# Optimization experiments

Hardware: AMD Instinct MI355X
Metric: run time of the kernel (lower is better)

Reference implementation:

```python
import jax, jax.numpy as jnp
import numpy as np
from jax import lax

K = 7            # pool_size / PSROI_BINS
C_OUT = 10       # output channels per bin (features has K*K*C_OUT channels)
FEAT_STRIDE = 16
LAMDA = 0.1
SAMPLES = 2      # bilinear sample points per bin side
H = W = 200
C_IN = K * K * C_OUT  # 490
N_ROIS = 512


def setup_inputs() -> dict:
    key = jax.random.key(0)
    k1, k2, k3, k4 = jax.random.split(key, 4)
    features = jax.random.normal(k1, (1, H, W, C_IN), jnp.float32)
    conv_w = jax.random.truncated_normal(k2, -2.0, 2.0, (3, 3, C_IN, 2 * K * K), jnp.float32) * 0.01
    img = H * FEAT_STRIDE  # image-space extent
    cxy = jax.random.uniform(k3, (N_ROIS, 2), minval=0.0, maxval=img - 1.0)
    wh = jax.random.uniform(k4, (N_ROIS, 2), minval=64.0, maxval=640.0)
    x1 = jnp.clip(cxy[:, 0] - wh[:, 0] * 0.5, 0.0, img - 2.0)
    y1 = jnp.clip(cxy[:, 1] - wh[:, 1] * 0.5, 0.0, img - 2.0)
    x2 = jnp.clip(x1 + wh[:, 0], x1 + 1.0, img - 1.0)
    y2 = jnp.clip(y1 + wh[:, 1], y1 + 1.0, img - 1.0)
    rois = jnp.stack([jnp.zeros(N_ROIS), x1, y1, x2, y2], axis=-1)  # [N,5]
    return {"features": features, "rois": rois, "conv_w": conv_w}


def _bilinear(feat, y, x):
    """feat [H,W,C]; y,x arbitrary equal shapes -> [..., C]."""
    Hf, Wf = feat.shape[0], feat.shape[1]
    y = jnp.clip(y, 0.0, Hf - 1.0)
    x = jnp.clip(x, 0.0, Wf - 1.0)
    y0 = jnp.floor(y)
    x0 = jnp.floor(x)
    y0i = y0.astype(jnp.int32)
    x0i = x0.astype(jnp.int32)
    y1i = jnp.minimum(y0i + 1, Hf - 1)
    x1i = jnp.minimum(x0i + 1, Wf - 1)
    wy = (y - y0)[..., None]
    wx = (x - x0)[..., None]
    v00 = feat[y0i, x0i]
    v01 = feat[y0i, x1i]
    v10 = feat[y1i, x0i]
    v11 = feat[y1i, x1i]
    return (v00 * (1 - wy) * (1 - wx) + v01 * (1 - wy) * wx
            + v10 * wy * (1 - wx) + v11 * wy * wx)


def _ps_roi(feat, box, cpg, offsets):
    """Position-sensitive RoI avg pooling with optional per-bin offsets.
    feat [H,W,K*K*cpg]; box (x1,y1,x2,y2) image coords; offsets [K,K,2] (dx,dy)
    in image coords or None. Returns [K,K,cpg]."""
    x1, y1, x2, y2 = box
    fx1 = x1 / FEAT_STRIDE
    fy1 = y1 / FEAT_STRIDE
    bw = (x2 - x1 + 1.0) / FEAT_STRIDE / K
    bh = (y2 - y1 + 1.0) / FEAT_STRIDE / K
    idx = jnp.arange(K, dtype=feat.dtype)
    s = (jnp.arange(SAMPLES, dtype=feat.dtype) + 0.5) / SAMPLES
    sx = fx1 + (idx[:, None] + s[None, :]) * bw  # [K(j), S]
    sy = fy1 + (idx[:, None] + s[None, :]) * bh  # [K(i), S]
    gx = jnp.broadcast_to(sx[None, :, None, :], (K, K, SAMPLES, SAMPLES))
    gy = jnp.broadcast_to(sy[:, None, :, None], (K, K, SAMPLES, SAMPLES))
    if offsets is not None:
        off = offsets / FEAT_STRIDE  # image -> feature coords
        gx = gx + off[..., 0][:, :, None, None]
        gy = gy + off[..., 1][:, :, None, None]
    vals = _bilinear(feat, gy, gx)                     # [K,K,S,S,K*K*cpg]
    vals = vals.reshape(K, K, SAMPLES, SAMPLES, K * K, cpg)
    bin_idx = (jnp.arange(K)[:, None] * K + jnp.arange(K)[None, :])  # [K,K]
    sel = jnp.take_along_axis(
        vals, bin_idx[:, :, None, None, None, None], axis=4)[..., 0, :]
    return sel.mean(axis=(2, 3))  # [K,K,cpg]


def reference(features, rois, conv_w):
    # 3x3 same conv producing 2*K*K offset channels (no bias)
    offset_map = lax.conv_general_dilated(
        features, conv_w, (1, 1), 'SAME',
        dimension_numbers=('NHWC', 'HWIO', 'NHWC'))[0]  # [H,W,2*K*K]
    feat0 = features[0]  # [H,W,K*K*C_OUT]

    def one_roi(roi):
        x1, y1, x2, y2 = roi[1], roi[2], roi[3], roi[4]
        rw = x2 - x1 + 1.0
        rh = y2 - y1 + 1.0
        box = (x1, y1, x2, y2)
        # stage 1: pool the offset map position-sensitively -> [K,K,2]
        off = _ps_roi(offset_map, box, 2, None).reshape(-1, 2)
        off = jnp.stack((off[:, 0] * rw * LAMDA,
                         off[:, 1] * rh * LAMDA), axis=-1).reshape(K, K, 2)
        # stage 2: deformable PS-RoI pooling of the features -> [K,K,C_OUT]
        return _ps_roi(feat0, box, C_OUT, off)

    return jax.vmap(one_roi)(rois)  # [N, K, K, C_OUT]
```

## Files before the change

### kernel.cpp

```cpp
#include <hip/hip_runtime.h>
#include <hip/hip_bf16.h>

#define Hh   200
#define Ww   200
#define CIN  490
#define OCN  98
#define KK   7
#define COUT 10
#define NROIS 512
#define PIX  8

#define PH   202
#define PW   202
#define PC   512
#define NPIX (Hh * Ww)
#define KCN  16
#define NF   7
#define NUNITS 144
#define HGRAN  18
#define HALF_SHORTS (8 * 3584)

typedef __attribute__((ext_vector_type(8))) short short8;
typedef __attribute__((ext_vector_type(4))) float float4v;

__global__ __launch_bounds__(256) void pack_feat_kernel(
    const float* __restrict__ feat, __hip_bfloat16* __restrict__ pf)
{
    int tid = blockIdx.x * 256 + threadIdx.x;
    if (tid >= PH * PW * (PC / 8)) return;
    int c8  = (tid & 63) * 8;
    int pix = tid >> 6;
    int py = pix / PW, px = pix % PW;
    __hip_bfloat16* dst = pf + (size_t)pix * PC + c8;
    bool interior = (py >= 1 && py <= Hh && px >= 1 && px <= Ww);

    __hip_bfloat16 v[8];
    if (interior && c8 + 8 <= CIN) {
        const float* s = feat + ((size_t)(py - 1) * Ww + (px - 1)) * CIN + c8;
#pragma unroll
        for (int q = 0; q < 4; ++q) {
            float2 f2 = *reinterpret_cast<const float2*>(s + q * 2);
            v[q * 2]     = __float2bfloat16(f2.x);
            v[q * 2 + 1] = __float2bfloat16(f2.y);
        }
    } else {
        const float* s = interior ? feat + ((size_t)(py - 1) * Ww + (px - 1)) * CIN : nullptr;
#pragma unroll
        for (int j = 0; j < 8; ++j) {
            float val = (interior && (c8 + j) < CIN) ? s[c8 + j] : 0.f;
            v[j] = __float2bfloat16(val);
        }
    }
    *reinterpret_cast<short8*>(dst) = *reinterpret_cast<short8*>(v);
}

__global__ __launch_bounds__(256) void pack_w_kernel(
    const float* __restrict__ w, __hip_bfloat16* __restrict__ bp)
{
    int idx = blockIdx.x * 256 + threadIdx.x;
    if (idx >= NUNITS * NF * 64 * 8) return;
    int j = idx & 7;
    int l = (idx >> 3) & 63;
    int f = (idx >> 9) % NF;
    int u = idx / (NF * 512);
    int kc = u / 9, tap = u % 9;
    int k = kc * 32 + ((l >> 4) * 8) + j;
    int n = f * 16 + (l & 15);
    float val = (k < CIN && n < OCN) ? w[((size_t)tap * CIN + k) * OCN + n] : 0.f;
    bp[idx] = __float2bfloat16(val);
}

__global__ __launch_bounds__(640) void conv_mfma_kernel(
    const short* __restrict__ pf,
    const short* __restrict__ bp,
    float* __restrict__ om)
{
    __shared__ short bsm[2 * HALF_SHORTS];

    int l = threadIdx.x & 63;
    int w = threadIdx.x >> 6;
    int mpos = w % 5;
    int ks = w / 5;
    int ubase = ks * 72;
    int m0 = blockIdx.x * 160 + mpos * 32;

    const short* abase0;
    const short* abase1;
    {
        int row0 = m0 + (l & 15);
        int row1 = m0 + 16 + (l & 15);
        int y0 = row0 / Ww, x0 = row0 % Ww;
        int y1 = row1 / Ww, x1 = row1 % Ww;
        abase0 = pf + ((size_t)(y0 * PW + x0) * PC) + ((l >> 4) * 8);
        abase1 = pf + ((size_t)(y1 * PW + x1) * PC) + ((l >> 4) * 8);
    }

    float4v acc[2][NF];
#pragma unroll
    for (int r = 0; r < 2; ++r)
#pragma unroll
        for (int f = 0; f < NF; ++f) acc[r][f] = (float4v){0.f, 0.f, 0.f, 0.f};

    auto aOff = [&](int u) -> int {
        int kc = u / 9, tap = u - kc * 9;
        int ky = tap / 3, kx = tap - ky * 3;
        return (ky * PW + kx) * PC + kc * 32;
    };
    int lbase = ks * HALF_SHORTS;

#pragma unroll
    for (int s = 0; s < 6; ++s) {
        int i = mpos + s * 5;
        if (i < 28) {
            int uu = ubase + i / 7, f = i % 7;
            short8 v = *reinterpret_cast<const short8*>(
                bp + ((size_t)(uu * NF + f)) * 512 + l * 8);
            *reinterpret_cast<short8*>(
                &bsm[lbase + (uu & 7) * 3584 + f * 512 + l * 8]) = v;
        }
    }
    short8 a00 = *reinterpret_cast<const short8*>(abase0 + aOff(ubase + 0));
    short8 a01 = *reinterpret_cast<const short8*>(abase0 + aOff(ubase + 1));
    short8 a02 = *reinterpret_cast<const short8*>(abase0 + aOff(ubase + 2));
    short8 a03 = *reinterpret_cast<const short8*>(abase0 + aOff(ubase + 3));
    short8 a10 = *reinterpret_cast<const short8*>(abase1 + aOff(ubase + 0));
    short8 a11 = *reinterpret_cast<const short8*>(abase1 + aOff(ubase + 1));
    short8 a12 = *reinterpret_cast<const short8*>(abase1 + aOff(ubase + 2));
    short8 a13 = *reinterpret_cast<const short8*>(abase1 + aOff(ubase + 3));
    __syncthreads();

    for (int g = 0; g < HGRAN; ++g) {
        bool more = (g < HGRAN - 1);
        int u0n = ubase + (g + 1) * 4;

        short8 st0, st1, st2, st3, st4, st5;
        int off0 = -1, off1 = -1, off2 = -1, off3 = -1, off4 = -1, off5 = -1;
        if (more) {
#define STAGE_LOAD(S, STV, OFFV)                                               \
            {                                                                  \
                int i = mpos + (S) * 5;                                        \
                if (i < 28) {                                                  \
                    int uu = u0n + i / 7, f = i % 7;                           \
                    STV = *reinterpret_cast<const short8*>(                    \
                        bp + ((size_t)(uu * NF + f)) * 512 + l * 8);           \
                    OFFV = lbase + (uu & 7) * 3584 + f * 512 + l * 8;          \
                }                                                              \
            }
            STAGE_LOAD(0, st0, off0)
            STAGE_LOAD(1, st1, off1)
            STAGE_LOAD(2, st2, off2)
            STAGE_LOAD(3, st3, off3)
            STAGE_LOAD(4, st4, off4)
            STAGE_LOAD(5, st5, off5)
#undef STAGE_LOAD
        }
        short8 n00, n01, n02, n03, n10, n11, n12, n13;
        if (more) {
            n00 = *reinterpret_cast<const short8*>(abase0 + aOff(u0n + 0));
            n01 = *reinterpret_cast<const short8*>(abase0 + aOff(u0n + 1));
            n02 = *reinterpret_cast<const short8*>(abase0 + aOff(u0n + 2));
            n03 = *reinterpret_cast<const short8*>(abase0 + aOff(u0n + 3));
            n10 = *reinterpret_cast<const short8*>(abase1 + aOff(u0n + 0));
            n11 = *reinterpret_cast<const short8*>(abase1 + aOff(u0n + 1));
            n12 = *reinterpret_cast<const short8*>(abase1 + aOff(u0n + 2));
            n13 = *reinterpret_cast<const short8*>(abase1 + aOff(u0n + 3));
        }

        int u0 = ubase + g * 4;
#define COMPUTE_UNIT(J, AR0, AR1)                                               \
        {                                                                       \
            int sbase = lbase + ((u0 + J) & 7) * 3584 + l * 8;                  \
            _Pragma("unroll")                                                   \
            for (int f = 0; f < NF; ++f) {                                      \
                short8 b = *reinterpret_cast<short8*>(&bsm[sbase + f * 512]);   \
                acc[0][f] = __builtin_amdgcn_mfma_f32_16x16x32_bf16(            \
                    AR0, b, acc[0][f], 0, 0, 0);                                \
                acc[1][f] = __builtin_amdgcn_mfma_f32_16x16x32_bf16(            \
                    AR1, b, acc[1][f], 0, 0, 0);                                \
            }                                                                   \
        }
        COMPUTE_UNIT(0, a00, a10)
        COMPUTE_UNIT(1, a01, a11)
        COMPUTE_UNIT(2, a02, a12)
        COMPUTE_UNIT(3, a03, a13)
#undef COMPUTE_UNIT

        if (off0 >= 0) *reinterpret_cast<short8*>(&bsm[off0]) = st0;
        if (off1 >= 0) *reinterpret_cast<short8*>(&bsm[off1]) = st1;
        if (off2 >= 0) *reinterpret_cast<short8*>(&bsm[off2]) = st2;
        if (off3 >= 0) *reinterpret_cast<short8*>(&bsm[off3]) = st3;
        if (off4 >= 0) *reinterpret_cast<short8*>(&bsm[off4]) = st4;
        if (off5 >= 0) *reinterpret_cast<short8*>(&bsm[off5]) = st5;
        if (more) {
            a00 = n00; a01 = n01; a02 = n02; a03 = n03;
            a10 = n10; a11 = n11; a12 = n12; a13 = n13;
        }
        __syncthreads();
    }

    float* lred = (float*)bsm;
    if (ks == 1) {
#pragma unroll
        for (int r = 0; r < 2; ++r)
#pragma unroll
            for (int f = 0; f < NF; ++f) {
                int idx = (((mpos * 2 + r) * NF + f) * 64 + l) * 4;
                *reinterpret_cast<float4v*>(&lred[idx]) = acc[r][f];
            }
    }
    __syncthreads();
    if (ks == 0) {
        int n = l & 15;
#pragma unroll
        for (int r = 0; r < 2; ++r) {
            int rbase = m0 + r * 16 + ((l >> 4) * 4);
#pragma unroll
            for (int f = 0; f < NF; ++f) {
                int idx = (((mpos * 2 + r) * NF + f) * 64 + l) * 4;
                float4v other = *reinterpret_cast<float4v*>(&lred[idx]);
                float4v tot = acc[r][f] + other;
                int col = f * 16 + n;
                if (col < OCN) {
#pragma unroll
                    for (int j = 0; j < 4; ++j)
                        om[(size_t)(rbase + j) * OCN + col] = tot[j];
                }
            }
        }
    }
}

__global__ __launch_bounds__(256) void conv3x3_kernel(
    const float* __restrict__ feat, const float* __restrict__ w,
    const float* __restrict__ zero, float* __restrict__ om)
{
    int idx = blockIdx.x * blockDim.x + threadIdx.x;
    if (idx >= Hh * (Ww / PIX) * OCN) return;
    int oc = idx % OCN;
    int g  = idx / OCN;
    int x0 = (g % (Ww / PIX)) * PIX;
    int y  = g / (Ww / PIX);

    float acc[PIX];
#pragma unroll
    for (int p = 0; p < PIX; ++p) acc[p] = 0.f;

    for (int ky = 0; ky < 3; ++ky) {
        int yy = y + ky - 1;
        if (yy < 0 || yy >= Hh) continue;
        const float* frow = feat + (size_t)yy * Ww * CIN;
        for (int kx = 0; kx < 3; ++kx) {
            const float* wp = w + ((ky * 3 + kx) * CIN) * OCN + oc;
            const float* fp[PIX];
#pragma unroll
            for (int p = 0; p < PIX; ++p) {
                int xx = x0 + p + kx - 1;
                fp[p] = (xx >= 0 && xx < Ww) ? (frow + (size_t)xx * CIN) : zero;
            }
            for (int ic = 0; ic < CIN; ic += 2) {
                float w0 = wp[ic * OCN];
                float w1 = wp[(ic + 1) * OCN];
#pragma unroll
                for (int p = 0; p < PIX; ++p) {
                    float2 f = *reinterpret_cast<const float2*>(fp[p] + ic);
                    acc[p] = fmaf(f.x, w0, acc[p]);
                    acc[p] = fmaf(f.y, w1, acc[p]);
                }
            }
        }
    }
    float* orow = om + ((size_t)y * Ww + x0) * OCN + oc;
#pragma unroll
    for (int p = 0; p < PIX; ++p) orow[p * OCN] = acc[p];
}

__device__ __forceinline__ void bilin_setup(float y, float x,
    int& i00, int& i01, int& i10, int& i11,
    float& w00, float& w01, float& w10, float& w11)
{
    y = fminf(fmaxf(y, 0.f), 199.f);
    x = fminf(fmaxf(x, 0.f), 199.f);
    float y0f = floorf(y), x0f = floorf(x);
    int y0 = (int)y0f, x0i = (int)x0f;
    int y1 = min(y0 + 1, 199), x1 = min(x0i + 1, 199);
    float wy = y - y0f, wx = x - x0f;
    i00 = y0 * Ww + x0i;  i01 = y0 * Ww + x1;
    i10 = y1 * Ww + x0i;  i11 = y1 * Ww + x1;
    w00 = (1.f - wy) * (1.f - wx);
    w01 = (1.f - wy) * wx;
    w10 = wy * (1.f - wx);
    w11 = wy * wx;
}

__global__ __launch_bounds__(256) void psroi_kernel(
    const float* __restrict__ feat, const float* __restrict__ rois,
    const float* __restrict__ om, float* __restrict__ out)
{
    int n = blockIdx.x;
    int t = threadIdx.x;

    float x1 = rois[n * 5 + 1], y1 = rois[n * 5 + 2];
    float x2 = rois[n * 5 + 3], y2 = rois[n * 5 + 4];
    float rw = x2 - x1 + 1.0f, rh = y2 - y1 + 1.0f;
    float fx1 = x1 * 0.0625f, fy1 = y1 * 0.0625f;
    float bw = (rw * 0.0625f) / 7.0f;
    float bh = (rh * 0.0625f) / 7.0f;

    __shared__ float offs[49][2];

    if (t < 49) {
        int bi = t / 7, bj = t % 7;
        float ax = 0.f, ay = 0.f;
#pragma unroll
        for (int ss = 0; ss < 4; ++ss) {
            float sj = ((float)(ss & 1) + 0.5f) * 0.5f;
            float si = ((float)(ss >> 1) + 0.5f) * 0.5f;
            float gx = fx1 + ((float)bj + sj) * bw;
            float gy = fy1 + ((float)bi + si) * bh;
            int i00, i01, i10, i11; float w00, w01, w10, w11;
            bilin_setup(gy, gx, i00, i01, i10, i11, w00, w01, w10, w11);
            int c0 = t * 2;
            const float* p00 = om + (size_t)i00 * OCN + c0;
            const float* p01 = om + (size_t)i01 * OCN + c0;
            const float* p10 = om + (size_t)i10 * OCN + c0;
            const float* p11 = om + (size_t)i11 * OCN + c0;
            ax += w00 * p00[0] + w01 * p01[0] + w10 * p10[0] + w11 * p11[0];
            ay += w00 * p00[1] + w01 * p01[1] + w10 * p10[1] + w11 * p11[1];
        }
        offs[t][0] = ax * 0.25f * rw * 0.1f * 0.0625f;
        offs[t][1] = ay * 0.25f * rh * 0.1f * 0.0625f;
    }
    __syncthreads();

    for (int o = t; o < KK * KK * COUT; o += blockDim.x) {
        int bin = o / COUT, c = o % COUT;
        int bi = bin / 7, bj = bin % 7;
        float dx = offs[bin][0], dy = offs[bin][1];
        int ch = bin * COUT + c;
        float acc = 0.f;
#pragma unroll
        for (int ss = 0; ss < 4; ++ss) {
            float sj = ((float)(ss & 1) + 0.5f) * 0.5f;
            float si = ((float)(ss >> 1) + 0.5f) * 0.5f;
            float gx = fx1 + ((float)bj + sj) * bw + dx;
            float gy = fy1 + ((float)bi + si) * bh + dy;
            int i00, i01, i10, i11; float w00, w01, w10, w11;
            bilin_setup(gy, gx, i00, i01, i10, i11, w00, w01, w10, w11);
            acc += w00 * feat[(size_t)i00 * CIN + ch]
                 + w01 * feat[(size_t)i01 * CIN + ch]
                 + w10 * feat[(size_t)i10 * CIN + ch]
                 + w11 * feat[(size_t)i11 * CIN + ch];
        }
        out[(size_t)n * (KK * KK * COUT) + o] = acc * 0.25f;
    }
}

extern "C" void kernel_launch(void* const* d_in, const int* in_sizes, int n_in,
                              void* d_out, int out_size, void* d_ws, size_t ws_size,
                              hipStream_t stream) {
    const float* feat = (const float*)d_in[0];
    const float* rois = (const float*)d_in[1];
    const float* w    = (const float*)d_in[2];
    float* out = (float*)d_out;

    const size_t OM_BYTES = (size_t)NPIX * OCN * 4;
    const size_t BP_BYTES = (size_t)NUNITS * NF * 64 * 8 * 2;
    const size_t PF_BYTES = (size_t)PH * PW * PC * 2;
    const size_t NEEDED = OM_BYTES + BP_BYTES + PF_BYTES;

    if (ws_size >= NEEDED) {
        float* om = (float*)d_ws;
        __hip_bfloat16* bp = (__hip_bfloat16*)((char*)d_ws + OM_BYTES);
        __hip_bfloat16* pf = (__hip_bfloat16*)((char*)d_ws + OM_BYTES + BP_BYTES);

        int wThreads = NUNITS * NF * 64 * 8;
        pack_w_kernel<<<(wThreads + 255) / 256, 256, 0, stream>>>(w, bp);
        int fThreads = PH * PW * (PC / 8);
        pack_feat_kernel<<<(fThreads + 255) / 256, 256, 0, stream>>>(feat, pf);
        conv_mfma_kernel<<<250, 640, 0, stream>>>(
            (const short*)pf, (const short*)bp, om);
        psroi_kernel<<<NROIS, 256, 0, stream>>>(feat, rois, om, out);
    } else {
        float* zero = (float*)d_ws;
        float* om   = (float*)d_ws + 1024;
        hipMemsetAsync(d_ws, 0, 4096, stream);
        int convThreads = Hh * (Ww / PIX) * OCN;
        conv3x3_kernel<<<(convThreads + 255) / 256, 256, 0, stream>>>(feat, w, zero, om);
        psroi_kernel<<<NROIS, 256, 0, stream>>>(feat, rois, om, out);
    }
}
```

Before: 108.6 us.

## Remap conv blocks per XCD, stream A-fragment loads, request two blocks per CU

The conv kernel now remaps blockIdx so that each XCD handles a contiguous range of row tiles, which is meant to improve L2 locality for the shared halo rows. The next A fragments are now loaded straight into the current registers right after each unit's MFMAs, replacing the separate prefetch register set, to cut VGPR pressure. The launch bounds now ask for a minimum of two blocks per CU. The shorter prefetch distance may expose more load latency, and the hard-coded 32/31 split assumes a grid of 250 blocks.

```diff
diff --git a/kernel.cpp b/kernel.cpp
--- a/kernel.cpp
+++ b/kernel.cpp
@@ -70,19 +70,24 @@
     bp[idx] = __float2bfloat16(val);
 }
 
-__global__ __launch_bounds__(640) void conv_mfma_kernel(
+__global__ __launch_bounds__(640, 2) void conv_mfma_kernel(
     const short* __restrict__ pf,
     const short* __restrict__ bp,
     float* __restrict__ om)
 {
     __shared__ short bsm[2 * HALF_SHORTS];
+
+    int orig = blockIdx.x;
+    int xcd = orig & 7;
+    int pos = orig >> 3;
+    int blk = ((xcd < 2) ? xcd * 32 : 64 + (xcd - 2) * 31) + pos;
 
     int l = threadIdx.x & 63;
     int w = threadIdx.x >> 6;
     int mpos = w % 5;
     int ks = w / 5;
     int ubase = ks * 72;
-    int m0 = blockIdx.x * 160 + mpos * 32;
+    int m0 = blk * 160 + mpos * 32;
 
     const short* abase0;
     const short* abase1;
@@ -154,20 +159,9 @@
             STAGE_LOAD(5, st5, off5)
 #undef STAGE_LOAD
         }
-        short8 n00, n01, n02, n03, n10, n11, n12, n13;
-        if (more) {
-            n00 = *reinterpret_cast<const short8*>(abase0 + aOff(u0n + 0));
-            n01 = *reinterpret_cast<const short8*>(abase0 + aOff(u0n + 1));
-            n02 = *reinterpret_cast<const short8*>(abase0 + aOff(u0n + 2));
-            n03 = *reinterpret_cast<const short8*>(abase0 + aOff(u0n + 3));
-            n10 = *reinterpret_cast<const short8*>(abase1 + aOff(u0n + 0));
-            n11 = *reinterpret_cast<const short8*>(abase1 + aOff(u0n + 1));
-            n12 = *reinterpret_cast<const short8*>(abase1 + aOff(u0n + 2));
-            n13 = *reinterpret_cast<const short8*>(abase1 + aOff(u0n + 3));
-        }
 
         int u0 = ubase + g * 4;
-#define COMPUTE_UNIT(J, AR0, AR1)                                               \
+#define UNIT_STEP(J, AR0, AR1)                                                  \
         {                                                                       \
             int sbase = lbase + ((u0 + J) & 7) * 3584 + l * 8;                  \
             _Pragma("unroll")                                                   \
@@ -178,12 +172,16 @@
                 acc[1][f] = __builtin_amdgcn_mfma_f32_16x16x32_bf16(            \
                     AR1, b, acc[1][f], 0, 0, 0);                                \
             }                                                                   \
-        }
-        COMPUTE_UNIT(0, a00, a10)
-        COMPUTE_UNIT(1, a01, a11)
-        COMPUTE_UNIT(2, a02, a12)
-        COMPUTE_UNIT(3, a03, a13)
-#undef COMPUTE_UNIT
+            if (more) {                                                         \
+                AR0 = *reinterpret_cast<const short8*>(abase0 + aOff(u0n + J)); \
+                AR1 = *reinterpret_cast<const short8*>(abase1 + aOff(u0n + J)); \
+            }                                                                   \
+        }
+        UNIT_STEP(0, a00, a10)
+        UNIT_STEP(1, a01, a11)
+        UNIT_STEP(2, a02, a12)
+        UNIT_STEP(3, a03, a13)
+#undef UNIT_STEP
 
         if (off0 >= 0) *reinterpret_cast<short8*>(&bsm[off0]) = st0;
         if (off1 >= 0) *reinterpret_cast<short8*>(&bsm[off1]) = st1;
@@ -191,10 +189,6 @@
         if (off3 >= 0) *reinterpret_cast<short8*>(&bsm[off3]) = st3;
         if (off4 >= 0) *reinterpret_cast<short8*>(&bsm[off4]) = st4;
         if (off5 >= 0) *reinterpret_cast<short8*>(&bsm[off5]) = st5;
-        if (more) {
-            a00 = n00; a01 = n01; a02 = n02; a03 = n03;
-            a10 = n10; a11 = n11; a12 = n12; a13 = n13;
-        }
         __syncthreads();
     }
 
```

After: 97.21 us. 1.12x faster.
